# Optimization experiments

Hardware: AMD Instinct MI355X
Metric: run time of the kernel (lower is better)

## Reference

```python
import jax, jax.numpy as jnp
import numpy as np

N = 100000   # nodes
H = 128      # hidden_size
T = 32       # transitivity_size
MD = 16      # mask_dim
K = 3        # propagation steps
E_S = 600000 # spatial edges
E_D = 600000 # dom edges


def setup_inputs() -> dict:
    key = jax.random.key(0)
    ks = jax.random.split(key, 12)
    return {
        "x": jax.random.normal(ks[0], (N, H), jnp.float32),
        "mask": jax.random.uniform(ks[1], (N, MD), jnp.float32),
        "spatial_edge_index": jax.random.randint(ks[2], (2, E_S), 0, N, jnp.int64 if jax.config.jax_enable_x64 else jnp.int32),
        "dom_edge_index": jax.random.randint(ks[3], (2, E_D), 0, N, jnp.int64 if jax.config.jax_enable_x64 else jnp.int32),
        "spatial_edge_attr": jax.random.normal(ks[4], (E_S, 4), jnp.float32),
        "dom_edge_attr": jax.random.normal(ks[5], (E_D, 1), jnp.float32),
        "W_trans": jax.random.normal(ks[6], (2 * H, T), jnp.float32) / np.sqrt(2 * H),
        "b_trans": jnp.zeros((T,), jnp.float32),
        "W_pos": jax.random.normal(ks[7], (4 + T, 1), jnp.float32) / np.sqrt(4 + T),
        "b_pos": jnp.zeros((1,), jnp.float32),
        "W_dom": jax.random.normal(ks[8], (1 + T, 1), jnp.float32) / np.sqrt(1 + T),
        "b_dom": jnp.zeros((1,), jnp.float32),
    }


def _edge_attrs(x, edge_index, W, b):
    # EdgeAttrs: gather src/dst node features, concat, linear + tanh -> [E, T]
    h = jnp.concatenate([x[edge_index[0]], x[edge_index[1]]], axis=1)
    return jnp.tanh(h @ W + b)


def _edge_mask(edge_attr, mask, edge_index, W, b, k_steps, n_nodes):
    # EdgeMask: per-edge gating weight in (0,1), then K rounds of
    # gate-weighted max-propagation of the node mask along edges.
    ew = jax.nn.sigmoid(edge_attr @ W + b)  # [E, 1]
    src, dst = edge_index[0], edge_index[1]
    m = mask
    for _ in range(k_steps):
        msg = m[src] * ew                                  # [E, MD]
        agg = jax.ops.segment_max(msg, dst, num_segments=n_nodes)
        m = jnp.maximum(m, agg)                            # -inf (empty segs) absorbed
    return m, ew


def reference(x, mask, spatial_edge_index, dom_edge_index, spatial_edge_attr,
              dom_edge_attr, W_trans, b_trans, W_pos, b_pos, W_dom, b_dom):
    n_nodes = x.shape[0]
    # spatial branch (projection is dom -> no safe_bc_edges broadcast)
    trans_s = _edge_attrs(x, spatial_edge_index, W_trans, b_trans)
    pos_in = jnp.concatenate([spatial_edge_attr, trans_s], axis=1)  # [E_S, 4+T]
    pos_mask, _pos_ew = _edge_mask(pos_in, mask, spatial_edge_index, W_pos, b_pos, K, n_nodes)
    # dom branch
    trans_d = _edge_attrs(x, dom_edge_index, W_trans, b_trans)
    dom_in = jnp.concatenate([dom_edge_attr, trans_d], axis=1)      # [E_D, 1+T]
    dom_mask, _dom_ew = _edge_mask(dom_in, mask, dom_edge_index, W_dom, b_dom, K, n_nodes)
    return jnp.maximum(mask, jnp.maximum(pos_mask, dom_mask))
```

## Files before the change

### kernel.cpp

```cpp
#include <hip/hip_runtime.h>
#include <hip/hip_bf16.h>
#include <stdint.h>

#define NNODES 100000
#define HID 128
#define TSZ 32
#define MDIM 16
#define ES 600000
#define ED 600000
#define ETOT (ES + ED)
#define GN (2 * NNODES)
#define GNP 200704
#define SCAN_BLOCKS 196
#define N16 (NNODES * MDIM)
#define NP8 (NNODES * 8)
#define GN8 (GN * 8)

typedef unsigned short ushort_t;

__device__ __forceinline__ float bflo(unsigned u) { return __uint_as_float(u << 16); }
__device__ __forceinline__ float bfhi(unsigned u) { return __uint_as_float(u & 0xffff0000u); }

__device__ __forceinline__ unsigned f2bf(float f) {
    unsigned u = __float_as_uint(f);
    return (u + 0x7FFFu + ((u >> 16) & 1u)) >> 16;
}
__device__ __forceinline__ unsigned packbf(float lo, float hi) {
    return f2bf(lo) | (f2bf(hi) << 16);
}

__device__ __forceinline__ float tanh_fast(float v) {
    float z = __expf(2.f * v);
    return 1.f - 2.f / (z + 1.f);
}

__global__ void k_init(const float* __restrict__ mask, unsigned* __restrict__ m_a,
                       int* __restrict__ counts) {
    int idx = blockIdx.x * 256 + threadIdx.x;
    if (idx < NP8) {
        float2 v = ((const float2*)mask)[idx];
        unsigned p = packbf(v.x, v.y);
        m_a[idx] = p;
        m_a[NP8 + idx] = p;
    }
    if (idx < GNP / 4) ((int4*)counts)[idx] = make_int4(0, 0, 0, 0);
}

__global__ __launch_bounds__(256) void k_pq(const float* __restrict__ x,
                                            const float* __restrict__ Wt,
                                            const float* __restrict__ bt,
                                            __hip_bfloat16* __restrict__ pq) {
    __shared__ float xs[64][132];
    __shared__ float wl[64][130];
    const int tid = threadIdx.x;
    const int n0 = blockIdx.x * 64;

    for (int i = tid; i < 4096; i += 256) {
        int h = i >> 5, c = i & 31;
        float a = Wt[i];
        float b = Wt[4096 + i];
        wl[c][h] = a;
        wl[c + 32][h] = b;
    }
    const float4* xsrc = (const float4*)(x + (size_t)n0 * 128);
#pragma unroll
    for (int i = 0; i < 8; ++i) {
        int idx = tid + 256 * i;
        int node = idx >> 5;
        int rem = idx & 31;
        if (n0 + node < NNODES) {
            float4 v = xsrc[idx];
            *(float4*)&xs[node][rem * 4] = v;
        }
    }
    __syncthreads();

    const int l = tid & 63;
    const int w = tid >> 6;
    const int c0 = l & 15;
    const int ng = w * 16 + (l >> 4) * 4;
    float acc[4][4] = {};
#pragma unroll 4
    for (int h = 0; h < 128; h += 2) {
        float2 xv[4], wv[4];
#pragma unroll
        for (int m = 0; m < 4; ++m) xv[m] = *(const float2*)&xs[ng + m][h];
#pragma unroll
        for (int m = 0; m < 4; ++m) wv[m] = *(const float2*)&wl[c0 + 16 * m][h];
#pragma unroll
        for (int a = 0; a < 4; ++a)
#pragma unroll
            for (int b = 0; b < 4; ++b)
                acc[a][b] = fmaf(xv[a].y, wv[b].y, fmaf(xv[a].x, wv[b].x, acc[a][b]));
    }
    float bv[4];
#pragma unroll
    for (int b = 0; b < 4; ++b) {
        int c = c0 + 16 * b;
        bv[b] = (c < 32) ? bt[c] : 0.f;
    }
#pragma unroll
    for (int a = 0; a < 4; ++a) {
        int node = n0 + ng + a;
        if (node < NNODES) {
#pragma unroll
            for (int b = 0; b < 4; ++b)
                pq[(size_t)node * 64 + c0 + 16 * b] = __float2bfloat16(acc[a][b] + bv[b]);
        }
    }
}

__global__ void k_count(const int* __restrict__ sdst, const int* __restrict__ ddst,
                        int* __restrict__ counts) {
    int e = blockIdx.x * 256 + threadIdx.x;
    if (e >= ETOT) return;
    int gd = (e < ES) ? sdst[e] : (ddst[e - ES] + NNODES);
    atomicAdd(&counts[gd], 1);
}

__global__ __launch_bounds__(256) void k_scan1(const int* __restrict__ counts,
                                               int* __restrict__ bsum) {
    __shared__ int sh[256];
    int tid = threadIdx.x;
    int4 v = ((const int4*)counts)[blockIdx.x * 256 + tid];
    sh[tid] = v.x + v.y + v.z + v.w;
    __syncthreads();
    for (int o = 128; o > 0; o >>= 1) {
        if (tid < o) sh[tid] += sh[tid + o];
        __syncthreads();
    }
    if (tid == 0) bsum[blockIdx.x] = sh[0];
}

__global__ __launch_bounds__(256) void k_scan2(const int* __restrict__ bsum,
                                               int* __restrict__ prefix) {
    __shared__ int sh[256];
    int tid = threadIdx.x;
    int v = (tid < SCAN_BLOCKS) ? bsum[tid] : 0;
    sh[tid] = v;
    __syncthreads();
    for (int o = 1; o < 256; o <<= 1) {
        int add = (tid >= o) ? sh[tid - o] : 0;
        __syncthreads();
        sh[tid] += add;
        __syncthreads();
    }
    prefix[tid] = sh[tid] - v;
}

__global__ __launch_bounds__(256) void k_scan3(const int* __restrict__ counts,
                                               const int* __restrict__ prefix,
                                               int* __restrict__ off,
                                               int* __restrict__ cursor) {
    __shared__ int sh[256];
    int tid = threadIdx.x;
    int4 v = ((const int4*)counts)[blockIdx.x * 256 + tid];
    int tot = v.x + v.y + v.z + v.w;
    sh[tid] = tot;
    __syncthreads();
    for (int o = 1; o < 256; o <<= 1) {
        int add = (tid >= o) ? sh[tid - o] : 0;
        __syncthreads();
        sh[tid] += add;
        __syncthreads();
    }
    int excl = sh[tid] - tot + prefix[blockIdx.x];
    int4 o4;
    o4.x = excl;
    o4.y = o4.x + v.x;
    o4.z = o4.y + v.y;
    o4.w = o4.z + v.z;
    ((int4*)off)[blockIdx.x * 256 + tid] = o4;
    ((int4*)cursor)[blockIdx.x * 256 + tid] = o4;
}

__global__ void k_ewfill(const ushort_t* __restrict__ pq,
                         const int* __restrict__ ssrc, const int* __restrict__ sdst,
                         const int* __restrict__ dsrc, const int* __restrict__ ddst,
                         const float* __restrict__ sattr, const float* __restrict__ dattr,
                         const float* __restrict__ Wp, const float* __restrict__ bp,
                         const float* __restrict__ Wd, const float* __restrict__ bd,
                         int* __restrict__ cursor, unsigned* __restrict__ csr) {
    int e = blockIdx.x * 256 + threadIdx.x;
    if (e >= ETOT) return;
    int src, dstg, srcg;
    float acc;
    const float* wt;
    if (e < ES) {
        src = ssrc[e];
        int dst = sdst[e];
        dstg = dst;
        srcg = src;
        const float4 a = *(const float4*)(sattr + (size_t)e * 4);
        acc = bp[0] + a.x * Wp[0] + a.y * Wp[1] + a.z * Wp[2] + a.w * Wp[3];
        wt = Wp + 4;
        const uint4* Pp = (const uint4*)(pq + (size_t)src * 64);
        const uint4* Qp = (const uint4*)(pq + (size_t)dst * 64 + 32);
#pragma unroll
        for (int c = 0; c < 4; ++c) {
            uint4 pu = Pp[c], qu = Qp[c];
            unsigned pw[4] = {pu.x, pu.y, pu.z, pu.w};
            unsigned qw[4] = {qu.x, qu.y, qu.z, qu.w};
#pragma unroll
            for (int k = 0; k < 4; ++k) {
                float v0 = bflo(pw[k]) + bflo(qw[k]);
                float v1 = bfhi(pw[k]) + bfhi(qw[k]);
                int t = c * 8 + k * 2;
                acc = fmaf(tanh_fast(v0), wt[t], acc);
                acc = fmaf(tanh_fast(v1), wt[t + 1], acc);
            }
        }
    } else {
        int ed = e - ES;
        src = dsrc[ed];
        int dst = ddst[ed];
        dstg = dst + NNODES;
        srcg = src + NNODES;
        acc = bd[0] + dattr[ed] * Wd[0];
        wt = Wd + 1;
        const uint4* Pp = (const uint4*)(pq + (size_t)src * 64);
        const uint4* Qp = (const uint4*)(pq + (size_t)dst * 64 + 32);
#pragma unroll
        for (int c = 0; c < 4; ++c) {
            uint4 pu = Pp[c], qu = Qp[c];
            unsigned pw[4] = {pu.x, pu.y, pu.z, pu.w};
            unsigned qw[4] = {qu.x, qu.y, qu.z, qu.w};
#pragma unroll
            for (int k = 0; k < 4; ++k) {
                float v0 = bflo(pw[k]) + bflo(qw[k]);
                float v1 = bfhi(pw[k]) + bfhi(qw[k]);
                int t = c * 8 + k * 2;
                acc = fmaf(tanh_fast(v0), wt[t], acc);
                acc = fmaf(tanh_fast(v1), wt[t + 1], acc);
            }
        }
    }
    float ew = 1.f / (1.f + __expf(-acc));
    unsigned entry = ((unsigned)srcg << 14) | (unsigned)(ew * 16383.f + 0.5f);
    int pos = atomicAdd(&cursor[dstg], 1);
    csr[pos] = entry;
}

__global__ void k_round(const unsigned* __restrict__ m_in, unsigned* __restrict__ m_out,
                        const int* __restrict__ off, const unsigned* __restrict__ csr) {
    int idx = blockIdx.x * 256 + threadIdx.x;
    if (idx >= GN8) return;
    int g = idx >> 3;
    int jp = idx & 7;
    int p0 = off[g], p1 = off[g + 1];
    unsigned cur = m_in[idx];
    float a = bflo(cur), b = bfhi(cur);
    int p = p0;
    for (; p + 1 < p1; p += 2) {
        unsigned e0 = csr[p], e1 = csr[p + 1];
        unsigned m0 = m_in[(e0 >> 14) * 8 + jp];
        unsigned m1 = m_in[(e1 >> 14) * 8 + jp];
        float w0 = (float)(e0 & 16383u) * (1.f / 16383.f);
        float w1 = (float)(e1 & 16383u) * (1.f / 16383.f);
        a = fmaxf(a, fmaxf(bflo(m0) * w0, bflo(m1) * w1));
        b = fmaxf(b, fmaxf(bfhi(m0) * w0, bfhi(m1) * w1));
    }
    if (p < p1) {
        unsigned e0 = csr[p];
        unsigned m0 = m_in[(e0 >> 14) * 8 + jp];
        float w0 = (float)(e0 & 16383u) * (1.f / 16383.f);
        a = fmaxf(a, bflo(m0) * w0);
        b = fmaxf(b, bfhi(m0) * w0);
    }
    m_out[idx] = packbf(a, b);
}

__global__ void k_round_final(const unsigned* __restrict__ m_in, float* __restrict__ out,
                              const int* __restrict__ off, const unsigned* __restrict__ csr) {
    int idx = blockIdx.x * 256 + threadIdx.x;
    if (idx >= NP8) return;
    int g = idx >> 3;
    int jp = idx & 7;
    float a, b;
    {
        unsigned cur = m_in[idx];
        a = bflo(cur); b = bfhi(cur);
        int p0 = off[g], p1 = off[g + 1];
        int p = p0;
        for (; p + 1 < p1; p += 2) {
            unsigned e0 = csr[p], e1 = csr[p + 1];
            unsigned m0 = m_in[(e0 >> 14) * 8 + jp];
            unsigned m1 = m_in[(e1 >> 14) * 8 + jp];
            float w0 = (float)(e0 & 16383u) * (1.f / 16383.f);
            float w1 = (float)(e1 & 16383u) * (1.f / 16383.f);
            a = fmaxf(a, fmaxf(bflo(m0) * w0, bflo(m1) * w1));
            b = fmaxf(b, fmaxf(bfhi(m0) * w0, bfhi(m1) * w1));
        }
        if (p < p1) {
            unsigned e0 = csr[p];
            unsigned m0 = m_in[(e0 >> 14) * 8 + jp];
            float w0 = (float)(e0 & 16383u) * (1.f / 16383.f);
            a = fmaxf(a, bflo(m0) * w0);
            b = fmaxf(b, bfhi(m0) * w0);
        }
    }
    {
        unsigned cur = m_in[NP8 + idx];
        float a2 = bflo(cur), b2 = bfhi(cur);
        int g2 = g + NNODES;
        int p0 = off[g2], p1 = off[g2 + 1];
        int p = p0;
        for (; p + 1 < p1; p += 2) {
            unsigned e0 = csr[p], e1 = csr[p + 1];
            unsigned m0 = m_in[(e0 >> 14) * 8 + jp];
            unsigned m1 = m_in[(e1 >> 14) * 8 + jp];
            float w0 = (float)(e0 & 16383u) * (1.f / 16383.f);
            float w1 = (float)(e1 & 16383u) * (1.f / 16383.f);
            a2 = fmaxf(a2, fmaxf(bflo(m0) * w0, bflo(m1) * w1));
            b2 = fmaxf(b2, fmaxf(bfhi(m0) * w0, bfhi(m1) * w1));
        }
        if (p < p1) {
            unsigned e0 = csr[p];
            unsigned m0 = m_in[(e0 >> 14) * 8 + jp];
            float w0 = (float)(e0 & 16383u) * (1.f / 16383.f);
            a2 = fmaxf(a2, bflo(m0) * w0);
            b2 = fmaxf(b2, bfhi(m0) * w0);
        }
        a = fmaxf(a, a2);
        b = fmaxf(b, b2);
    }
    *(float2*)&out[g * 16 + jp * 2] = make_float2(a, b);
}

extern "C" void kernel_launch(void* const* d_in, const int* in_sizes, int n_in,
                              void* d_out, int out_size, void* d_ws, size_t ws_size,
                              hipStream_t stream) {
    const float* x     = (const float*)d_in[0];
    const float* mask  = (const float*)d_in[1];
    const int*   sei   = (const int*)d_in[2];
    const int*   dei   = (const int*)d_in[3];
    const float* sattr = (const float*)d_in[4];
    const float* dattr = (const float*)d_in[5];
    const float* Wt    = (const float*)d_in[6];
    const float* bt    = (const float*)d_in[7];
    const float* Wp    = (const float*)d_in[8];
    const float* bp    = (const float*)d_in[9];
    const float* Wd    = (const float*)d_in[10];
    const float* bd    = (const float*)d_in[11];
    float* out = (float*)d_out;

    char* ws = (char*)d_ws;
    size_t o = 0;
    auto take = [&](size_t bytes) -> char* {
        char* p = ws + o;
        o = (o + bytes + 255) & ~(size_t)255;
        return p;
    };
    __hip_bfloat16* pq = (__hip_bfloat16*)take((size_t)NNODES * 64 * 2);
    int* counts  = (int*)take((size_t)GNP * 4);
    int* off     = (int*)take((size_t)GNP * 4);
    int* cursor  = (int*)take((size_t)GNP * 4);
    int* bsum    = (int*)take(256 * 4);
    int* prefix  = (int*)take(256 * 4);
    unsigned* csr = (unsigned*)take((size_t)ETOT * 4);
    unsigned* m_a = (unsigned*)take((size_t)GN8 * 4);
    unsigned* m_b = (unsigned*)take((size_t)GN8 * 4);

    k_init<<<3125, 256, 0, stream>>>(mask, m_a, counts);
    k_pq<<<(NNODES + 63) / 64, 256, 0, stream>>>(x, Wt, bt, pq);
    k_count<<<(ETOT + 255) / 256, 256, 0, stream>>>(sei + ES, dei + ED, counts);
    k_scan1<<<SCAN_BLOCKS, 256, 0, stream>>>(counts, bsum);
    k_scan2<<<1, 256, 0, stream>>>(bsum, prefix);
    k_scan3<<<SCAN_BLOCKS, 256, 0, stream>>>(counts, prefix, off, cursor);
    k_ewfill<<<(ETOT + 255) / 256, 256, 0, stream>>>((const ushort_t*)pq,
        sei, sei + ES, dei, dei + ED, sattr, dattr, Wp, bp, Wd, bd, cursor, csr);
    k_round<<<(GN8 + 255) / 256, 256, 0, stream>>>(m_a, m_b, off, csr);
    k_round<<<(GN8 + 255) / 256, 256, 0, stream>>>(m_b, m_a, off, csr);
    k_round_final<<<(NP8 + 255) / 256, 256, 0, stream>>>(m_a, out, off, csr);
}
```

Baseline: 352.3 us.

## Quantize PQ projections to int8 and split propagation rounds per branch

```diff
diff --git a/kernel.cpp b/kernel.cpp
--- a/kernel.cpp
+++ b/kernel.cpp
@@ -15,6 +15,7 @@
 #define N16 (NNODES * MDIM)
 #define NP8 (NNODES * 8)
 #define GN8 (GN * 8)
+#define PQ_BLOCKS 1563
 
 typedef unsigned short ushort_t;
 
@@ -49,7 +50,7 @@
 __global__ __launch_bounds__(256) void k_pq(const float* __restrict__ x,
                                             const float* __restrict__ Wt,
                                             const float* __restrict__ bt,
-                                            __hip_bfloat16* __restrict__ pq) {
+                                            char* __restrict__ pq) {
     __shared__ float xs[64][132];
     __shared__ float wl[64][130];
     const int tid = threadIdx.x;
@@ -99,15 +100,21 @@
         int c = c0 + 16 * b;
         bv[b] = (c < 32) ? bt[c] : 0.f;
     }
+    __syncthreads();
+    char* buf = (char*)&xs[0][0];
 #pragma unroll
     for (int a = 0; a < 4; ++a) {
-        int node = n0 + ng + a;
-        if (node < NNODES) {
-#pragma unroll
-            for (int b = 0; b < 4; ++b)
-                pq[(size_t)node * 64 + c0 + 16 * b] = __float2bfloat16(acc[a][b] + bv[b]);
-        }
-    }
+#pragma unroll
+        for (int b = 0; b < 4; ++b) {
+            float v = acc[a][b] + bv[b];
+            int q = __float2int_rn(v * 32.f);
+            q = max(-127, min(127, q));
+            buf[(ng + a) * 64 + c0 + 16 * b] = (char)q;
+        }
+    }
+    __syncthreads();
+    uint4 v4 = ((const uint4*)buf)[tid];
+    ((uint4*)(pq + (size_t)blockIdx.x * 4096))[tid] = v4;
 }
 
 __global__ void k_count(const int* __restrict__ sdst, const int* __restrict__ ddst,
@@ -174,7 +181,7 @@
     ((int4*)cursor)[blockIdx.x * 256 + tid] = o4;
 }
 
-__global__ void k_ewfill(const ushort_t* __restrict__ pq,
+__global__ void k_ewfill(const char* __restrict__ pq,
                          const int* __restrict__ ssrc, const int* __restrict__ sdst,
                          const int* __restrict__ dsrc, const int* __restrict__ ddst,
                          const float* __restrict__ sattr, const float* __restrict__ dattr,
@@ -183,56 +190,41 @@
                          int* __restrict__ cursor, unsigned* __restrict__ csr) {
     int e = blockIdx.x * 256 + threadIdx.x;
     if (e >= ETOT) return;
-    int src, dstg, srcg;
+    int src, dst, dstg, srcg;
     float acc;
     const float* wt;
     if (e < ES) {
         src = ssrc[e];
-        int dst = sdst[e];
+        dst = sdst[e];
         dstg = dst;
         srcg = src;
         const float4 a = *(const float4*)(sattr + (size_t)e * 4);
         acc = bp[0] + a.x * Wp[0] + a.y * Wp[1] + a.z * Wp[2] + a.w * Wp[3];
         wt = Wp + 4;
-        const uint4* Pp = (const uint4*)(pq + (size_t)src * 64);
-        const uint4* Qp = (const uint4*)(pq + (size_t)dst * 64 + 32);
-#pragma unroll
-        for (int c = 0; c < 4; ++c) {
-            uint4 pu = Pp[c], qu = Qp[c];
-            unsigned pw[4] = {pu.x, pu.y, pu.z, pu.w};
-            unsigned qw[4] = {qu.x, qu.y, qu.z, qu.w};
-#pragma unroll
-            for (int k = 0; k < 4; ++k) {
-                float v0 = bflo(pw[k]) + bflo(qw[k]);
-                float v1 = bfhi(pw[k]) + bfhi(qw[k]);
-                int t = c * 8 + k * 2;
-                acc = fmaf(tanh_fast(v0), wt[t], acc);
-                acc = fmaf(tanh_fast(v1), wt[t + 1], acc);
-            }
-        }
     } else {
         int ed = e - ES;
         src = dsrc[ed];
-        int dst = ddst[ed];
+        dst = ddst[ed];
         dstg = dst + NNODES;
         srcg = src + NNODES;
         acc = bd[0] + dattr[ed] * Wd[0];
         wt = Wd + 1;
-        const uint4* Pp = (const uint4*)(pq + (size_t)src * 64);
-        const uint4* Qp = (const uint4*)(pq + (size_t)dst * 64 + 32);
-#pragma unroll
-        for (int c = 0; c < 4; ++c) {
-            uint4 pu = Pp[c], qu = Qp[c];
-            unsigned pw[4] = {pu.x, pu.y, pu.z, pu.w};
-            unsigned qw[4] = {qu.x, qu.y, qu.z, qu.w};
-#pragma unroll
-            for (int k = 0; k < 4; ++k) {
-                float v0 = bflo(pw[k]) + bflo(qw[k]);
-                float v1 = bfhi(pw[k]) + bfhi(qw[k]);
-                int t = c * 8 + k * 2;
-                acc = fmaf(tanh_fast(v0), wt[t], acc);
-                acc = fmaf(tanh_fast(v1), wt[t + 1], acc);
-            }
+    }
+    const uint4* Pp = (const uint4*)(pq + (size_t)src * 64);
+    const uint4* Qp = (const uint4*)(pq + (size_t)dst * 64 + 32);
+    uint4 pa = Pp[0], pb = Pp[1];
+    uint4 qa = Qp[0], qb = Qp[1];
+    unsigned pw[8] = {pa.x, pa.y, pa.z, pa.w, pb.x, pb.y, pb.z, pb.w};
+    unsigned qw[8] = {qa.x, qa.y, qa.z, qa.w, qb.x, qb.y, qb.z, qb.w};
+#pragma unroll
+    for (int d = 0; d < 8; ++d) {
+        unsigned a = pw[d], b = qw[d];
+#pragma unroll
+        for (int k = 0; k < 4; ++k) {
+            int pi = (int)(char)(a >> (8 * k));
+            int qi = (int)(char)(b >> (8 * k));
+            float t = tanh_fast((float)(pi + qi) * 0.03125f);
+            acc = fmaf(t, wt[d * 4 + k], acc);
         }
     }
     float ew = 1.f / (1.f + __expf(-acc));
@@ -242,13 +234,15 @@
 }
 
 __global__ void k_round(const unsigned* __restrict__ m_in, unsigned* __restrict__ m_out,
-                        const int* __restrict__ off, const unsigned* __restrict__ csr) {
+                        const int* __restrict__ off, const unsigned* __restrict__ csr,
+                        int base) {
     int idx = blockIdx.x * 256 + threadIdx.x;
-    if (idx >= GN8) return;
-    int g = idx >> 3;
+    if (idx >= NP8) return;
+    int g = base + (idx >> 3);
     int jp = idx & 7;
+    int mi = base * 8 + idx;
     int p0 = off[g], p1 = off[g + 1];
-    unsigned cur = m_in[idx];
+    unsigned cur = m_in[mi];
     float a = bflo(cur), b = bfhi(cur);
     int p = p0;
     for (; p + 1 < p1; p += 2) {
@@ -267,7 +261,7 @@
         a = fmaxf(a, bflo(m0) * w0);
         b = fmaxf(b, bfhi(m0) * w0);
     }
-    m_out[idx] = packbf(a, b);
+    m_out[mi] = packbf(a, b);
 }
 
 __global__ void k_round_final(const unsigned* __restrict__ m_in, float* __restrict__ out,
@@ -351,7 +345,7 @@
         o = (o + bytes + 255) & ~(size_t)255;
         return p;
     };
-    __hip_bfloat16* pq = (__hip_bfloat16*)take((size_t)NNODES * 64 * 2);
+    char* pq     = take((size_t)PQ_BLOCKS * 4096);
     int* counts  = (int*)take((size_t)GNP * 4);
     int* off     = (int*)take((size_t)GNP * 4);
     int* cursor  = (int*)take((size_t)GNP * 4);
@@ -362,14 +356,16 @@
     unsigned* m_b = (unsigned*)take((size_t)GN8 * 4);
 
     k_init<<<3125, 256, 0, stream>>>(mask, m_a, counts);
-    k_pq<<<(NNODES + 63) / 64, 256, 0, stream>>>(x, Wt, bt, pq);
+    k_pq<<<PQ_BLOCKS, 256, 0, stream>>>(x, Wt, bt, pq);
     k_count<<<(ETOT + 255) / 256, 256, 0, stream>>>(sei + ES, dei + ED, counts);
     k_scan1<<<SCAN_BLOCKS, 256, 0, stream>>>(counts, bsum);
     k_scan2<<<1, 256, 0, stream>>>(bsum, prefix);
     k_scan3<<<SCAN_BLOCKS, 256, 0, stream>>>(counts, prefix, off, cursor);
-    k_ewfill<<<(ETOT + 255) / 256, 256, 0, stream>>>((const ushort_t*)pq,
+    k_ewfill<<<(ETOT + 255) / 256, 256, 0, stream>>>(pq,
         sei, sei + ES, dei, dei + ED, sattr, dattr, Wp, bp, Wd, bd, cursor, csr);
-    k_round<<<(GN8 + 255) / 256, 256, 0, stream>>>(m_a, m_b, off, csr);
-    k_round<<<(GN8 + 255) / 256, 256, 0, stream>>>(m_b, m_a, off, csr);
-    k_round_final<<<(NP8 + 255) / 256, 256, 0, stream>>>(m_a, out, off, csr);
-}
+    k_round<<<3125, 256, 0, stream>>>(m_a, m_b, off, csr, 0);
+    k_round<<<3125, 256, 0, stream>>>(m_a, m_b, off, csr, NNODES);
+    k_round<<<3125, 256, 0, stream>>>(m_b, m_a, off, csr, 0);
+    k_round<<<3125, 256, 0, stream>>>(m_b, m_a, off, csr, NNODES);
+    k_round_final<<<3125, 256, 0, stream>>>(m_a, out, off, csr);
+}
```

Result: faster. 342.2 us (-2.9%).
